# Performance work log

Measured on AMD Instinct MI355X. Metric: run time of the kernel, lower is better.

The kernel has to match this reference:

```python
import jax, jax.numpy as jnp
import numpy as np

C = 128
K = 5
M = 150000   # num vertices
NF = 300000  # num faces
D = 192      # volume side
NEG_SLOPE = 0.2


def _x_shift(K):
    # Exactly replicates the torch module's grid construction.
    grid = np.linspace(-K // 2, K // 2, K)
    grid_3d = np.stack(np.meshgrid(grid, grid, grid), axis=0).transpose(2, 1, 3, 0)
    return jnp.asarray(grid_3d.reshape(-1, 3), jnp.float32)  # [K^3, 3]


def _trilinear_border(vol, g):
    # vol: [D1, D2, D3]; g: [N, 3] normalized coords in (x, y, z) order
    # (x -> D3/W, y -> D2/H, z -> D1/D), align_corners=True, padding_mode='border'.
    D1, D2, D3 = vol.shape
    def pix(c, S):
        return jnp.clip((c + 1.0) * 0.5 * (S - 1), 0.0, S - 1.0)
    ix, iy, iz = pix(g[:, 0], D3), pix(g[:, 1], D2), pix(g[:, 2], D1)
    x0f, y0f, z0f = jnp.floor(ix), jnp.floor(iy), jnp.floor(iz)
    wx, wy, wz = ix - x0f, iy - y0f, iz - z0f
    x0 = x0f.astype(jnp.int32); y0 = y0f.astype(jnp.int32); z0 = z0f.astype(jnp.int32)
    x1 = jnp.minimum(x0 + 1, D3 - 1)
    y1 = jnp.minimum(y0 + 1, D2 - 1)
    z1 = jnp.minimum(z0 + 1, D1 - 1)
    c000 = vol[z0, y0, x0]; c001 = vol[z0, y0, x1]
    c010 = vol[z0, y1, x0]; c011 = vol[z0, y1, x1]
    c100 = vol[z1, y0, x0]; c101 = vol[z1, y0, x1]
    c110 = vol[z1, y1, x0]; c111 = vol[z1, y1, x1]
    c00 = c000 * (1 - wx) + c001 * wx
    c01 = c010 * (1 - wx) + c011 * wx
    c10 = c100 * (1 - wx) + c101 * wx
    c11 = c110 * (1 - wx) + c111 * wx
    c0 = c00 * (1 - wy) + c01 * wy
    c1 = c10 * (1 - wy) + c11 * wy
    return c0 * (1 - wz) + c1 * wz


def _leaky(x):
    return jnp.where(x >= 0, x, NEG_SLOPE * x)


def setup_inputs() -> dict:
    key = jax.random.key(0)
    ks = jax.random.split(key, 9)
    v = jax.random.uniform(ks[0], (1, M, 3), jnp.float32, -0.9, 0.9)
    f = jax.random.randint(ks[1], (1, NF, 3), 0, M, jnp.int32)
    V = jax.random.normal(ks[2], (1, 1, D, D, D), jnp.float32)
    def init(k, shape, fan):
        return jax.random.normal(k, shape, jnp.float32) / np.sqrt(fan).astype(np.float32)
    Wconv = init(ks[3], (C, 1, K, K, K), K ** 3)
    bconv = jnp.zeros((C,), jnp.float32)
    Wlfc = init(ks[4], (C, C), C)
    blfc = jnp.zeros((C,), jnp.float32)
    W1 = init(ks[5], (C, 6), 6)
    b1 = jnp.zeros((C,), jnp.float32)
    W2 = init(ks[6], (4 * C, 2 * C), 2 * C)
    b2 = jnp.zeros((4 * C,), jnp.float32)
    W3 = init(ks[7], (2 * C, 4 * C), 4 * C)
    b3 = jnp.zeros((2 * C,), jnp.float32)
    return dict(v=v, f=f, V=V, Wconv=Wconv, bconv=bconv, Wlfc=Wlfc, blfc=blfc,
                W1=W1, b1=b1, W2=W2, b2=b2, W3=W3, b3=b3)


def reference(v, f, V, Wconv, bconv, Wlfc, blfc, W1, b1, W2, b2, W3, b3):
    m = v.shape[1]
    D1, D2, D3 = V.shape[2], V.shape[3], V.shape[4]
    Dm = max(D1, D2, D3)
    rescale = jnp.array([D3 / Dm, D2 / Dm, D1 / Dm], jnp.float32)
    x_shift = _x_shift(K)  # [K^3, 3]

    # --- cube sampling (Q = n_scale = 1), done under no_grad in torch ---
    pts = (v[0][:, None, :] + x_shift / Dm * 2.0) / rescale  # [m, K^3, 3]
    cubes = _trilinear_border(V[0, 0], pts.reshape(-1, 3)).reshape(m, K ** 3)
    cubes = jax.lax.stop_gradient(cubes)

    # --- localconv: Conv3d with full-size kernel == GEMM over flattened cube ---
    z_local = cubes @ Wconv.reshape(C, -1).T + bconv      # [m, C]
    z_local = _leaky(z_local)
    z_local = _leaky(z_local @ Wlfc.T + blfc)             # [m, C]

    # --- vertex normals (area-weighted face-normal accumulation, pytorch3d style) ---
    faces = f[0]
    vv = v[0]
    p0, p1, p2 = vv[faces[:, 0]], vv[faces[:, 1]], vv[faces[:, 2]]
    fn = jnp.cross(p1 - p0, p2 - p0)
    vn = jnp.zeros_like(vv)
    vn = vn.at[faces[:, 0]].add(fn).at[faces[:, 1]].add(fn).at[faces[:, 2]].add(fn)
    vn = vn / jnp.maximum(jnp.linalg.norm(vn, axis=-1, keepdims=True), 1e-6)

    # --- point-wise MLP fusion ---
    x = jnp.concatenate([v, vn[None]], axis=2)            # [1, m, 6]
    z_point = _leaky(x @ W1.T + b1)                       # [1, m, C]
    z = jnp.concatenate([z_point, z_local[None]], axis=2) # [1, m, 2C]
    z = _leaky(z @ W2.T + b2)                             # [1, m, 4C]
    z = _leaky(z @ W3.T + b3)                             # [1, m, 2C]
    return z
```

## Files before the change

### kernel.cpp

```cpp
#include <hip/hip_runtime.h>
#include <hip/hip_fp16.h>

#define NEG_SLOPE 0.2f

using f16x8 = __attribute__((ext_vector_type(8))) _Float16;
using f32x4 = __attribute__((ext_vector_type(4))) float;

__device__ __forceinline__ float leakyf(float x) { return x >= 0.f ? x : NEG_SLOPE * x; }

__device__ __forceinline__ void gload_lds16(const void* g, void* l) {
    __builtin_amdgcn_global_load_lds(
        (const __attribute__((address_space(1))) unsigned int*)g,
        (__attribute__((address_space(3))) unsigned int*)l, 16, 0, 0);
}

#define MFMA16(a, b, c) __builtin_amdgcn_mfma_f32_16x16x32_f16(a, b, c, 0, 0, 0)

__global__ __launch_bounds__(256)
void fn_kernel(const float* __restrict__ v, const int* __restrict__ f,
               float4* __restrict__ fn4, int nf) {
    int i = blockIdx.x * 256 + threadIdx.x;
    if (i >= nf) return;
    int i0 = f[3 * i], i1 = f[3 * i + 1], i2 = f[3 * i + 2];
    float p0x = v[3 * i0], p0y = v[3 * i0 + 1], p0z = v[3 * i0 + 2];
    float ux = v[3 * i1] - p0x, uy = v[3 * i1 + 1] - p0y, uz = v[3 * i1 + 2] - p0z;
    float wx = v[3 * i2] - p0x, wy = v[3 * i2 + 1] - p0y, wz = v[3 * i2 + 2] - p0z;
    fn4[i] = make_float4(uy * wz - uz * wy, uz * wx - ux * wz, ux * wy - uy * wx, 0.f);
}

__global__ __launch_bounds__(256)
void inc_hist_kernel(const int* __restrict__ f, unsigned* __restrict__ gh, int NE) {
    __shared__ unsigned h[1024];
    const int t = threadIdx.x, blk = blockIdx.x;
    h[t] = 0; h[t + 256] = 0; h[t + 512] = 0; h[t + 768] = 0;
    __syncthreads();
    int base = blk * 4096;
#pragma unroll
    for (int k = 0; k < 16; ++k) {
        int idx = base + k * 256 + t;
        if (idx < NE) atomicAdd(&h[((unsigned)f[idx]) >> 8], 1u);
    }
    __syncthreads();
#pragma unroll
    for (int k = 0; k < 4; ++k) { int b = t + k * 256; gh[(size_t)blk * 1024 + b] = h[b]; }
}

__global__ __launch_bounds__(256)
void row_scan_kernel(unsigned* __restrict__ gh, unsigned* __restrict__ binTotals, int NB) {
    __shared__ unsigned s[256];
    __shared__ unsigned carrySh;
    const int bin = blockIdx.x, t = threadIdx.x;
    if (t == 0) carrySh = 0;
    __syncthreads();
    for (int base = 0; base < NB; base += 256) {
        unsigned c = carrySh;
        int i = base + t;
        unsigned val = (i < NB) ? gh[(size_t)i * 1024 + bin] : 0;
        s[t] = val;
        __syncthreads();
        for (int d = 1; d < 256; d <<= 1) {
            unsigned x = (t >= d) ? s[t - d] : 0;
            __syncthreads();
            s[t] += x;
            __syncthreads();
        }
        if (i < NB) gh[(size_t)i * 1024 + bin] = s[t] - val + c;
        if (t == 255) carrySh = c + s[255];
        __syncthreads();
    }
    if (t == 0) binTotals[bin] = carrySh;
}

__global__ __launch_bounds__(1024)
void bin_scan_kernel(const unsigned* __restrict__ binTotals, unsigned* __restrict__ binstart) {
    __shared__ unsigned s[1024];
    int t = threadIdx.x;
    unsigned val = binTotals[t];
    s[t] = val;
    __syncthreads();
    for (int d = 1; d < 1024; d <<= 1) {
        unsigned x = (t >= d) ? s[t - d] : 0;
        __syncthreads();
        s[t] += x;
        __syncthreads();
    }
    binstart[t] = s[t] - val;
    if (t == 1023) binstart[1024] = s[1023];
}

__global__ __launch_bounds__(256)
void inc_scatter_kernel(const int* __restrict__ f, const unsigned* __restrict__ gh,
                        const unsigned* __restrict__ binstart,
                        unsigned* __restrict__ sortedV, unsigned* __restrict__ sortedE,
                        int NE) {
    __shared__ unsigned loc[1024];
    const int t = threadIdx.x, blk = blockIdx.x;
#pragma unroll
    for (int k = 0; k < 4; ++k) {
        int b = t + k * 256;
        loc[b] = gh[(size_t)blk * 1024 + b] + binstart[b];
    }
    __syncthreads();
    int base = blk * 4096;
#pragma unroll
    for (int k = 0; k < 16; ++k) {
        int idx = base + k * 256 + t;
        if (idx < NE) {
            unsigned vv = (unsigned)f[idx];
            unsigned pos = atomicAdd(&loc[vv >> 8], 1u);
            sortedV[pos] = vv;
            sortedE[pos] = (unsigned)idx;
        }
    }
}

__global__ __launch_bounds__(256)
void vn_gather_kernel(const unsigned* __restrict__ sortedV, const unsigned* __restrict__ sortedE,
                      const float4* __restrict__ fn4, const unsigned* __restrict__ binstart,
                      float* __restrict__ vn, int M) {
    __shared__ float acc[768];
    const int t = threadIdx.x, b = blockIdx.x;
    acc[t] = 0.f; acc[t + 256] = 0.f; acc[t + 512] = 0.f;
    __syncthreads();
    unsigned s = binstart[b], e = binstart[b + 1];
    for (unsigned i = s + t; i < e; i += 256) {
        unsigned vv = sortedV[i];
        float4 fn = fn4[sortedE[i] / 3];
        int lv = (int)(vv & 255u) * 3;
        atomicAdd(&acc[lv + 0], fn.x);
        atomicAdd(&acc[lv + 1], fn.y);
        atomicAdd(&acc[lv + 2], fn.z);
    }
    __syncthreads();
    int gv = b * 256 + t;
    if (gv < M) {
        vn[3 * gv + 0] = acc[t * 3 + 0];
        vn[3 * gv + 1] = acc[t * 3 + 1];
        vn[3 * gv + 2] = acc[t * 3 + 2];
    }
}

__global__ __launch_bounds__(256)
void code_hist_kernel(const float* __restrict__ v, int* __restrict__ codes,
                      int* __restrict__ hist, int M) {
    int i = blockIdx.x * 256 + threadIdx.x;
    if (i >= M) return;
    int cx = min(max((int)((v[3 * i + 0] + 1.f) * 8.f), 0), 15);
    int cy = min(max((int)((v[3 * i + 1] + 1.f) * 8.f), 0), 15);
    int cz = min(max((int)((v[3 * i + 2] + 1.f) * 8.f), 0), 15);
    int code = 0;
#pragma unroll
    for (int b = 0; b < 4; ++b)
        code |= (((cx >> b) & 1) << (3 * b)) | (((cy >> b) & 1) << (3 * b + 1)) |
                (((cz >> b) & 1) << (3 * b + 2));
    codes[i] = code;
    atomicAdd(&hist[code], 1);
}

__global__ __launch_bounds__(1024)
void scan_kernel(const int* __restrict__ hist, int* __restrict__ offs) {
    __shared__ int s[1024];
    int t = threadIdx.x;
    int v0 = hist[4 * t], v1 = hist[4 * t + 1], v2 = hist[4 * t + 2], v3 = hist[4 * t + 3];
    int sum = v0 + v1 + v2 + v3;
    s[t] = sum;
    __syncthreads();
    for (int d = 1; d < 1024; d <<= 1) {
        int val = (t >= d) ? s[t - d] : 0;
        __syncthreads();
        s[t] += val;
        __syncthreads();
    }
    int excl = s[t] - sum;
    offs[4 * t + 0] = excl;
    offs[4 * t + 1] = excl + v0;
    offs[4 * t + 2] = excl + v0 + v1;
    offs[4 * t + 3] = excl + v0 + v1 + v2;
}

__global__ __launch_bounds__(256)
void scatter_kernel(const int* __restrict__ codes, int* __restrict__ offs,
                    int* __restrict__ perm, int M) {
    int i = blockIdx.x * 256 + threadIdx.x;
    if (i >= M) return;
    int pos = atomicAdd(&offs[codes[i]], 1);
    perm[pos] = i;
}

__global__ __launch_bounds__(256)
void sample_kernel(const float* __restrict__ v, const float* __restrict__ vol,
                   const int* __restrict__ perm,
                   __half* __restrict__ cubes, int m_start, int cnt, int nwg) {
    __shared__ float bbox[2][392];
    __shared__ int pi0[2][16];
    __shared__ float pw[2][16];
    const int half = threadIdx.x >> 7;
    const int q = threadIdx.x & 127;
    int q8 = nwg >> 3, r8 = nwg & 7;
    int xcd = blockIdx.x & 7, idxb = blockIdx.x >> 3;
    int bid = (xcd < r8 ? xcd * (q8 + 1) : r8 * (q8 + 1) + (xcd - r8) * q8) + idxb;
    int ml = bid * 2 + half;
    bool valid = ml < cnt;
    int m = valid ? perm[m_start + ml] : 0;

    if (valid && q < 15) {
        int axis = q / 5, idx = q - 5 * axis;
        float g = -3.f + 1.25f * (float)idx;
        float p = v[3 * m + axis] + g / 192.f * 2.f;
        float pos = fminf(fmaxf((p + 1.f) * 0.5f * 191.f, 0.f), 191.f);
        float fl = floorf(pos);
        pi0[half][q] = (int)fl;
        pw[half][q] = pos - fl;
    }
    __syncthreads();
    if (valid) {
        int xlo = pi0[half][0], ylo = pi0[half][5], zlo = pi0[half][10];
        for (int i = q; i < 392; i += 128) {
            int dx = i & 7;
            int dy = (i >> 3) % 7;
            int dz = i / 56;
            int X = min(xlo + dx, 191), Y = min(ylo + dy, 191), Z = min(zlo + dz, 191);
            bbox[half][i] = vol[Z * 36864 + Y * 192 + X];
        }
    }
    __syncthreads();
    if (!valid) return;
    __half* dst = cubes + (size_t)ml * 128;
    if (q >= 125) { dst[q] = __float2half(0.f); return; }
    int a = q % 5, b = (q / 5) % 5, c = q / 25;
    int xlo = pi0[half][0], ylo = pi0[half][5], zlo = pi0[half][10];
    int gx0 = pi0[half][a], gy0 = pi0[half][5 + b], gz0 = pi0[half][10 + c];
    float wxv = pw[half][a], wyv = pw[half][5 + b], wzv = pw[half][10 + c];
    int x0 = gx0 - xlo, y0 = gy0 - ylo, z0 = gz0 - zlo;
    int x1 = min(gx0 + 1, 191) - xlo;
    int y1 = min(gy0 + 1, 191) - ylo;
    int z1 = min(gz0 + 1, 191) - zlo;
    const float* bb = bbox[half];
    int b00 = (z0 * 7 + y0) * 8, b01 = (z0 * 7 + y1) * 8;
    int b10 = (z1 * 7 + y0) * 8, b11 = (z1 * 7 + y1) * 8;
    float c000 = bb[b00 + x0], c001 = bb[b00 + x1];
    float c010 = bb[b01 + x0], c011 = bb[b01 + x1];
    float c100 = bb[b10 + x0], c101 = bb[b10 + x1];
    float c110 = bb[b11 + x0], c111 = bb[b11 + x1];
    float omx = 1.f - wxv, omy = 1.f - wyv, omz = 1.f - wzv;
    float c00 = c000 * omx + c001 * wxv;
    float c01 = c010 * omx + c011 * wxv;
    float c10 = c100 * omx + c101 * wxv;
    float c11 = c110 * omx + c111 * wxv;
    float c0 = c00 * omy + c01 * wyv;
    float c1 = c10 * omy + c11 * wyv;
    dst[25 * a + 5 * b + c] = __float2half(c0 * omz + c1 * wzv);
}

__global__ __launch_bounds__(256)
void prep_weights(const float* __restrict__ Wconv, const float* __restrict__ Wlfc,
                  const float* __restrict__ W2, const float* __restrict__ W3,
                  __half* __restrict__ wpadh, __half* __restrict__ wlfch,
                  __half* __restrict__ w2h, __half* __restrict__ w3h) {
    int b = blockIdx.x, t = threadIdx.x;
    if (b < 64) {
        int i = b * 256 + t; int ch = i >> 7, k = i & 127;
        wpadh[i] = __float2half(k < 125 ? Wconv[ch * 125 + k] : 0.f);
    } else if (b < 128) {
        int i = (b - 64) * 256 + t; wlfch[i] = __float2half(Wlfc[i]);
    } else if (b < 640) {
        int i = (b - 128) * 256 + t; w2h[i] = __float2half(W2[i]);
    } else {
        int i = (b - 640) * 256 + t; w3h[i] = __float2half(W3[i]);
    }
}

__global__ __launch_bounds__(256)
void point_kernel(const float* __restrict__ v, const float* __restrict__ vn,
                  const int* __restrict__ perm,
                  const float* __restrict__ W1, const float* __restrict__ b1,
                  __half* __restrict__ zcat, int m_start, int cnt) {
    int ml = blockIdx.x * 2 + (threadIdx.x >> 7);
    if (ml >= cnt) return;
    int n = threadIdx.x & 127;
    int m = perm[m_start + ml];
    float x0 = v[3 * m], x1 = v[3 * m + 1], x2 = v[3 * m + 2];
    float nx = vn[3 * m], ny = vn[3 * m + 1], nz = vn[3 * m + 2];
    float nrm = fmaxf(sqrtf(nx * nx + ny * ny + nz * nz), 1e-6f);
    nx /= nrm; ny /= nrm; nz /= nrm;
    const float* w = W1 + n * 6;
    float z = b1[n] + x0 * w[0] + x1 * w[1] + x2 * w[2] + nx * w[3] + ny * w[4] + nz * w[5];
    zcat[(size_t)ml * 256 + n] = __float2half(leakyf(z));
}

__global__ __launch_bounds__(256)
void convlfc_kernel(const __half* __restrict__ cubes, const __half* __restrict__ wconvh,
                    const float* __restrict__ bconv, const __half* __restrict__ wlfch,
                    const float* __restrict__ blfc, __half* __restrict__ zcat) {
    __shared__ __half Zt[128 * 128];
    __shared__ __half As[128 * 64];
    __shared__ __half Bs[128 * 64];
    const int t = threadIdx.x;
    const int lane = t & 63, wave = t >> 6;
    const int lr = lane & 15, lg = lane >> 4;
    const int wm = wave >> 1, wn = wave & 1;
    const int m0 = blockIdx.x * 128;
    const int srow = t >> 3;
    const int scb = ((t & 7) << 4) ^ (((t >> 3) & 7) << 4);
    const int swz = (lr & 7) << 4;

    const __half* Ag = cubes + (size_t)(m0 + srow) * 128 + (scb >> 1);
    const __half* Bg = wconvh + (size_t)srow * 128 + (scb >> 1);
    __half* Al = As + wave * 512;
    __half* Bl = Bs + wave * 512;
    const char* aB = (const char*)As + (wm * 64 + lr) * 128;
    const char* bB = (const char*)Bs + (wn * 64 + lr) * 128;

    f32x4 acc[4][4] = {};
    for (int kc = 0; kc < 128; kc += 64) {
#pragma unroll
        for (int i = 0; i < 4; ++i) {
            gload_lds16(Ag + (size_t)i * 32 * 128 + kc, Al + i * 2048);
            gload_lds16(Bg + (size_t)i * 32 * 128 + kc, Bl + i * 2048);
        }
        __syncthreads();
#pragma unroll
        for (int kk = 0; kk < 2; ++kk) {
            const int ko = (kk * 64 + lg * 16) ^ swz;
            f16x8 af[4], bf[4];
#pragma unroll
            for (int fx = 0; fx < 4; ++fx) {
                af[fx] = *(const f16x8*)(aB + fx * 2048 + ko);
                bf[fx] = *(const f16x8*)(bB + fx * 2048 + ko);
            }
#pragma unroll
            for (int fm = 0; fm < 4; ++fm)
#pragma unroll
                for (int fn = 0; fn < 4; ++fn)
                    acc[fm][fn] = MFMA16(af[fm], bf[fn], acc[fm][fn]);
        }
        __syncthreads();
    }
#pragma unroll
    for (int fm = 0; fm < 4; ++fm) {
#pragma unroll
        for (int fn = 0; fn < 4; ++fn) {
            int col = wn * 64 + fn * 16 + lr;
            float bias = bconv[col];
#pragma unroll
            for (int r = 0; r < 4; ++r) {
                int row = wm * 64 + fm * 16 + lg * 4 + r;
                float val = leakyf(acc[fm][fn][r] + bias);
                *(__half*)((char*)Zt + row * 256 + ((2 * col) ^ ((row & 7) << 4))) = __float2half(val);
            }
        }
    }
    __syncthreads();

    const __half* Bg2 = wlfch + (size_t)srow * 128 + (scb >> 1);
    const char* zR = (const char*)Zt + (wm * 64 + lr) * 256;
    f32x4 acc2[4][4] = {};
    for (int kc = 0; kc < 128; kc += 64) {
#pragma unroll
        for (int i = 0; i < 4; ++i)
            gload_lds16(Bg2 + (size_t)i * 32 * 128 + kc, Bl + i * 2048);
        __syncthreads();
#pragma unroll
        for (int kk = 0; kk < 2; ++kk) {
            const int kb = kc * 2 + kk * 64 + lg * 16;
            const int ko = (kk * 64 + lg * 16) ^ swz;
            f16x8 af[4], bf[4];
#pragma unroll
            for (int fx = 0; fx < 4; ++fx) {
                af[fx] = *(const f16x8*)(zR + fx * 4096 + (kb ^ swz));
                bf[fx] = *(const f16x8*)(bB + fx * 2048 + ko);
            }
#pragma unroll
            for (int fm = 0; fm < 4; ++fm)
#pragma unroll
                for (int fn = 0; fn < 4; ++fn)
                    acc2[fm][fn] = MFMA16(af[fm], bf[fn], acc2[fm][fn]);
        }
        __syncthreads();
    }
#pragma unroll
    for (int fm = 0; fm < 4; ++fm) {
#pragma unroll
        for (int fn = 0; fn < 4; ++fn) {
            int col = wn * 64 + fn * 16 + lr;
            float bias = blfc[col];
#pragma unroll
            for (int r = 0; r < 4; ++r) {
                int row = m0 + wm * 64 + fm * 16 + lg * 4 + r;
                zcat[(size_t)row * 256 + 128 + col] = __float2half(leakyf(acc2[fm][fn][r] + bias));
            }
        }
    }
}

template<bool F32OUT>
__global__ __launch_bounds__(256)
void gemm_mfma(const __half* __restrict__ A, const __half* __restrict__ W,
               const float* __restrict__ bias, void* __restrict__ outp,
               int K, int Meff, int OS, int OC, const int* __restrict__ rowmap) {
    __shared__ __half As[8192];
    __shared__ __half Bs[8192];
    const int t = threadIdx.x;
    const int lane = t & 63, wave = t >> 6;
    const int lr = lane & 15, lg = lane >> 4;
    const int wm = wave >> 1, wn = wave & 1;
    const int m0 = blockIdx.x * 128, n0 = blockIdx.y * 128;

    const int srow = t >> 3;
    const int scb = ((t & 7) << 4) ^ (((t >> 3) & 7) << 4);
    const __half* Ag = A + (size_t)(m0 + srow) * K + (scb >> 1);
    const __half* Wg = W + (size_t)(n0 + srow) * K + (scb >> 1);
    __half* Al = As + wave * 512;
    __half* Bl = Bs + wave * 512;

    const int swz = (lr & 7) << 4;
    const char* aB = (const char*)As + (wm * 64 + lr) * 128;
    const char* bB = (const char*)Bs + (wn * 64 + lr) * 128;
    const int k0 = (lg * 16) ^ swz;
    const int k1 = (64 + lg * 16) ^ swz;

    f32x4 acc[4][4] = {};

    for (int kc = 0; kc < K; kc += 64) {
#pragma unroll
        for (int i = 0; i < 4; ++i) {
            gload_lds16(Ag + (size_t)i * 32 * K + kc, Al + i * 2048);
            gload_lds16(Wg + (size_t)i * 32 * K + kc, Bl + i * 2048);
        }
        __syncthreads();
        f16x8 af[4], bf[4];
#pragma unroll
        for (int fx = 0; fx < 4; ++fx) {
            af[fx] = *(const f16x8*)(aB + fx * 2048 + k0);
            bf[fx] = *(const f16x8*)(bB + fx * 2048 + k0);
        }
#pragma unroll
        for (int fm = 0; fm < 4; ++fm)
#pragma unroll
            for (int fn = 0; fn < 4; ++fn)
                acc[fm][fn] = MFMA16(af[fm], bf[fn], acc[fm][fn]);
#pragma unroll
        for (int fx = 0; fx < 4; ++fx) {
            af[fx] = *(const f16x8*)(aB + fx * 2048 + k1);
            bf[fx] = *(const f16x8*)(bB + fx * 2048 + k1);
        }
#pragma unroll
        for (int fm = 0; fm < 4; ++fm)
#pragma unroll
            for (int fn = 0; fn < 4; ++fn)
                acc[fm][fn] = MFMA16(af[fm], bf[fn], acc[fm][fn]);
        __syncthreads();
    }

    float bv[4];
#pragma unroll
    for (int fn = 0; fn < 4; ++fn) bv[fn] = bias[n0 + wn * 64 + fn * 16 + lr];
    const int rbase = m0 + wm * 64 + lg * 4;
    const int cbase = OC + n0 + wn * 64 + lr;
#pragma unroll
    for (int fm = 0; fm < 4; ++fm) {
#pragma unroll
        for (int r = 0; r < 4; ++r) {
            int row = rbase + fm * 16 + r;
            if (row < Meff) {
                size_t orow = (size_t)(rowmap ? rowmap[row] : row);
#pragma unroll
                for (int fn = 0; fn < 4; ++fn) {
                    float val = leakyf(acc[fm][fn][r] + bv[fn]);
                    if (F32OUT)
                        ((float*)outp)[orow * OS + cbase + fn * 16] = val;
                    else
                        ((__half*)outp)[orow * OS + cbase + fn * 16] = __float2half(val);
                }
            }
        }
    }
}

extern "C" void kernel_launch(void* const* d_in, const int* in_sizes, int n_in,
                              void* d_out, int out_size, void* d_ws, size_t ws_size,
                              hipStream_t stream) {
    const float* v = (const float*)d_in[0];
    const int* f = (const int*)d_in[1];
    const float* vol = (const float*)d_in[2];
    const float* Wconv = (const float*)d_in[3];
    const float* bconv = (const float*)d_in[4];
    const float* Wlfc = (const float*)d_in[5];
    const float* blfc = (const float*)d_in[6];
    const float* W1 = (const float*)d_in[7];
    const float* b1 = (const float*)d_in[8];
    const float* W2 = (const float*)d_in[9];
    const float* b2 = (const float*)d_in[10];
    const float* W3 = (const float*)d_in[11];
    const float* b3 = (const float*)d_in[12];
    float* out = (float*)d_out;
    const int M = in_sizes[0] / 3;
    const int NF = in_sizes[1] / 3;
    const int NE = 3 * NF;
    const int NB = (NE + 4095) / 4096;

    char* base = (char*)d_ws;
    float* vn = (float*)base;
    size_t off = ((size_t)M * 12 + 255) & ~(size_t)255;
    int* codes = (int*)(base + off); off += ((size_t)M * 4 + 255) & ~(size_t)255;
    int* perm  = (int*)(base + off); off += ((size_t)M * 4 + 255) & ~(size_t)255;
    int* hist  = (int*)(base + off); off += 4096 * 4;
    int* offs  = (int*)(base + off); off += 4096 * 4;
    float4* fn4 = (float4*)(base + off); off += (size_t)NF * 16;
    unsigned* sortedV = (unsigned*)(base + off); off += ((size_t)NE * 4 + 255) & ~(size_t)255;
    unsigned* sortedE = (unsigned*)(base + off); off += ((size_t)NE * 4 + 255) & ~(size_t)255;
    unsigned* gh = (unsigned*)(base + off); off += ((size_t)1024 * NB * 4 + 255) & ~(size_t)255;
    unsigned* binstart = (unsigned*)(base + off); off += 1032 * 4;
    unsigned* binTotals = (unsigned*)(base + off); off += 1024 * 4;
    __half* wpadh = (__half*)(base + off); off += 32768;
    __half* wlfch = (__half*)(base + off); off += 32768;
    __half* w2h = (__half*)(base + off); off += 262144;
    __half* w3h = (__half*)(base + off); off += 262144;
    size_t avail = ws_size > off ? ws_size - off : 0;
    size_t Mpad = ((size_t)M + 127) & ~(size_t)127;
    size_t chm = (avail / 1792) & ~(size_t)127;
    if (chm > Mpad) chm = Mpad;
    if (chm < 128) chm = 128;
    __half* cubes = (__half*)(base + off);
    __half* zcat = cubes + chm * 128;
    __half* h = zcat + chm * 256;

    fn_kernel<<<(NF + 255) / 256, 256, 0, stream>>>(v, f, fn4, NF);
    inc_hist_kernel<<<NB, 256, 0, stream>>>(f, gh, NE);
    row_scan_kernel<<<1024, 256, 0, stream>>>(gh, binTotals, NB);
    bin_scan_kernel<<<1, 1024, 0, stream>>>(binTotals, binstart);
    inc_scatter_kernel<<<NB, 256, 0, stream>>>(f, gh, binstart, sortedV, sortedE, NE);
    vn_gather_kernel<<<(M + 255) / 256, 256, 0, stream>>>(sortedV, sortedE, fn4, binstart, vn, M);

    hipMemsetAsync(hist, 0, 4096 * 4, stream);
    code_hist_kernel<<<(M + 255) / 256, 256, 0, stream>>>(v, codes, hist, M);
    scan_kernel<<<1, 1024, 0, stream>>>(hist, offs);
    scatter_kernel<<<(M + 255) / 256, 256, 0, stream>>>(codes, offs, perm, M);
    prep_weights<<<1152, 256, 0, stream>>>(Wconv, Wlfc, W2, W3, wpadh, wlfch, w2h, w3h);

    for (size_t ms = 0; ms < (size_t)M; ms += chm) {
        size_t rem = (size_t)M - ms;
        int cnt = (int)(rem < chm ? rem : chm);
        int mb = (cnt + 127) / 128;
        int nblk = (cnt + 1) / 2;
        sample_kernel<<<nblk, 256, 0, stream>>>(v, vol, perm, cubes, (int)ms, cnt, nblk);
        convlfc_kernel<<<mb, 256, 0, stream>>>(cubes, wpadh, bconv, wlfch, blfc, zcat);
        point_kernel<<<(cnt + 1) / 2, 256, 0, stream>>>(v, vn, perm, W1, b1, zcat, (int)ms, cnt);
        gemm_mfma<false><<<dim3(mb, 4), 256, 0, stream>>>(zcat, w2h, b2, h, 256, mb * 128, 512, 0, nullptr);
        gemm_mfma<true><<<dim3(mb, 2), 256, 0, stream>>>(h, w3h, b3, out, 512, cnt, 256, 0, perm + ms);
    }
}
```

Measured before the change: 518.7 us.

## Widen GEMM N-tile to 256 and restructure sample bbox load layout

The MLP GEMMs now compute 128x256 tiles per block, with each wave holding 4x8 MFMA accumulators. This halves the grid along N and reuses each A tile across twice as many output columns, at the cost of more registers and LDS per block and lower occupancy. Separately, the sampling kernel's bounding-box gather now uses a fixed (dy,dx) mapping per thread with a z loop. It stores rows with a stride of 9 floats instead of 8, aiming to cut integer div/mod work and LDS bank conflicts.

```diff
diff --git a/kernel.cpp b/kernel.cpp
--- a/kernel.cpp
+++ b/kernel.cpp
@@ -191,7 +191,7 @@
 void sample_kernel(const float* __restrict__ v, const float* __restrict__ vol,
                    const int* __restrict__ perm,
                    __half* __restrict__ cubes, int m_start, int cnt, int nwg) {
-    __shared__ float bbox[2][392];
+    __shared__ float bbox[2][448];
     __shared__ int pi0[2][16];
     __shared__ float pw[2][16];
     const int half = threadIdx.x >> 7;
@@ -215,12 +215,21 @@
     __syncthreads();
     if (valid) {
         int xlo = pi0[half][0], ylo = pi0[half][5], zlo = pi0[half][10];
-        for (int i = q; i < 392; i += 128) {
-            int dx = i & 7;
-            int dy = (i >> 3) % 7;
-            int dz = i / 56;
-            int X = min(xlo + dx, 191), Y = min(ylo + dy, 191), Z = min(zlo + dz, 191);
-            bbox[half][i] = vol[Z * 36864 + Y * 192 + X];
+        int j = q & 63;
+        int dy = j >> 3, dx = j & 7;
+        if (dy < 7) {
+            int X = min(xlo + dx, 191);
+            int Y = min(ylo + dy, 191);
+            int rowoff = dy * 9 + dx;
+            const float* volYX = vol + Y * 192 + X;
+#pragma unroll
+            for (int k = 0; k < 4; ++k) {
+                int pz = (q >> 6) + k * 2;
+                if (pz < 7) {
+                    int Z = min(zlo + pz, 191);
+                    bbox[half][pz * 63 + rowoff] = volYX[Z * 36864];
+                }
+            }
         }
     }
     __syncthreads();
@@ -236,8 +245,8 @@
     int y1 = min(gy0 + 1, 191) - ylo;
     int z1 = min(gz0 + 1, 191) - zlo;
     const float* bb = bbox[half];
-    int b00 = (z0 * 7 + y0) * 8, b01 = (z0 * 7 + y1) * 8;
-    int b10 = (z1 * 7 + y0) * 8, b11 = (z1 * 7 + y1) * 8;
+    int b00 = z0 * 63 + y0 * 9, b01 = z0 * 63 + y1 * 9;
+    int b10 = z1 * 63 + y0 * 9, b11 = z1 * 63 + y1 * 9;
     float c000 = bb[b00 + x0], c001 = bb[b00 + x1];
     float c010 = bb[b01 + x0], c011 = bb[b01 + x1];
     float c100 = bb[b10 + x0], c101 = bb[b10 + x1];
@@ -395,16 +404,16 @@
 
 template<bool F32OUT>
 __global__ __launch_bounds__(256)
-void gemm_mfma(const __half* __restrict__ A, const __half* __restrict__ W,
+void gemm_bigm(const __half* __restrict__ A, const __half* __restrict__ W,
                const float* __restrict__ bias, void* __restrict__ outp,
                int K, int Meff, int OS, int OC, const int* __restrict__ rowmap) {
     __shared__ __half As[8192];
-    __shared__ __half Bs[8192];
+    __shared__ __half Bs[16384];
     const int t = threadIdx.x;
     const int lane = t & 63, wave = t >> 6;
     const int lr = lane & 15, lg = lane >> 4;
     const int wm = wave >> 1, wn = wave & 1;
-    const int m0 = blockIdx.x * 128, n0 = blockIdx.y * 128;
+    const int m0 = blockIdx.x * 128, n0 = blockIdx.y * 256;
 
     const int srow = t >> 3;
     const int scb = ((t & 7) << 4) ^ (((t >> 3) & 7) << 4);
@@ -415,48 +424,44 @@
 
     const int swz = (lr & 7) << 4;
     const char* aB = (const char*)As + (wm * 64 + lr) * 128;
-    const char* bB = (const char*)Bs + (wn * 64 + lr) * 128;
+    const char* bB = (const char*)Bs + (wn * 128 + lr) * 128;
     const int k0 = (lg * 16) ^ swz;
     const int k1 = (64 + lg * 16) ^ swz;
 
-    f32x4 acc[4][4] = {};
+    f32x4 acc[4][8] = {};
 
     for (int kc = 0; kc < K; kc += 64) {
 #pragma unroll
-        for (int i = 0; i < 4; ++i) {
+        for (int i = 0; i < 4; ++i)
             gload_lds16(Ag + (size_t)i * 32 * K + kc, Al + i * 2048);
+#pragma unroll
+        for (int i = 0; i < 8; ++i)
             gload_lds16(Wg + (size_t)i * 32 * K + kc, Bl + i * 2048);
-        }
-        __syncthreads();
-        f16x8 af[4], bf[4];
-#pragma unroll
-        for (int fx = 0; fx < 4; ++fx) {
-            af[fx] = *(const f16x8*)(aB + fx * 2048 + k0);
-            bf[fx] = *(const f16x8*)(bB + fx * 2048 + k0);
-        }
-#pragma unroll
-        for (int fm = 0; fm < 4; ++fm)
-#pragma unroll
-            for (int fn = 0; fn < 4; ++fn)
-                acc[fm][fn] = MFMA16(af[fm], bf[fn], acc[fm][fn]);
-#pragma unroll
-        for (int fx = 0; fx < 4; ++fx) {
-            af[fx] = *(const f16x8*)(aB + fx * 2048 + k1);
-            bf[fx] = *(const f16x8*)(bB + fx * 2048 + k1);
-        }
-#pragma unroll
-        for (int fm = 0; fm < 4; ++fm)
-#pragma unroll
-            for (int fn = 0; fn < 4; ++fn)
-                acc[fm][fn] = MFMA16(af[fm], bf[fn], acc[fm][fn]);
-        __syncthreads();
-    }
-
-    float bv[4];
-#pragma unroll
-    for (int fn = 0; fn < 4; ++fn) bv[fn] = bias[n0 + wn * 64 + fn * 16 + lr];
+        __syncthreads();
+#pragma unroll
+        for (int kk = 0; kk < 2; ++kk) {
+            const int ko = (kk == 0) ? k0 : k1;
+            f16x8 af[4], bf[8];
+#pragma unroll
+            for (int fm = 0; fm < 4; ++fm)
+                af[fm] = *(const f16x8*)(aB + fm * 2048 + ko);
+#pragma unroll
+            for (int fn = 0; fn < 8; ++fn)
+                bf[fn] = *(const f16x8*)(bB + fn * 2048 + ko);
+#pragma unroll
+            for (int fm = 0; fm < 4; ++fm)
+#pragma unroll
+                for (int fn = 0; fn < 8; ++fn)
+                    acc[fm][fn] = MFMA16(af[fm], bf[fn], acc[fm][fn]);
+        }
+        __syncthreads();
+    }
+
+    float bv[8];
+#pragma unroll
+    for (int fn = 0; fn < 8; ++fn) bv[fn] = bias[n0 + wn * 128 + fn * 16 + lr];
     const int rbase = m0 + wm * 64 + lg * 4;
-    const int cbase = OC + n0 + wn * 64 + lr;
+    const int cbase = OC + n0 + wn * 128 + lr;
 #pragma unroll
     for (int fm = 0; fm < 4; ++fm) {
 #pragma unroll
@@ -465,7 +470,7 @@
             if (row < Meff) {
                 size_t orow = (size_t)(rowmap ? rowmap[row] : row);
 #pragma unroll
-                for (int fn = 0; fn < 4; ++fn) {
+                for (int fn = 0; fn < 8; ++fn) {
                     float val = leakyf(acc[fm][fn][r] + bv[fn]);
                     if (F32OUT)
                         ((float*)outp)[orow * OS + cbase + fn * 16] = val;
@@ -546,7 +551,9 @@
         sample_kernel<<<nblk, 256, 0, stream>>>(v, vol, perm, cubes, (int)ms, cnt, nblk);
         convlfc_kernel<<<mb, 256, 0, stream>>>(cubes, wpadh, bconv, wlfch, blfc, zcat);
         point_kernel<<<(cnt + 1) / 2, 256, 0, stream>>>(v, vn, perm, W1, b1, zcat, (int)ms, cnt);
-        gemm_mfma<false><<<dim3(mb, 4), 256, 0, stream>>>(zcat, w2h, b2, h, 256, mb * 128, 512, 0, nullptr);
-        gemm_mfma<true><<<dim3(mb, 2), 256, 0, stream>>>(h, w3h, b3, out, 512, cnt, 256, 0, perm + ms);
-    }
-}
+        gemm_bigm<false><<<dim3(mb, 2), 256, 0, stream>>>(
+            zcat, w2h, b2, h, 256, mb * 128, 512, 0, nullptr);
+        gemm_bigm<true><<<dim3(mb, 1), 256, 0, stream>>>(
+            h, w3h, b3, out, 512, cnt, 256, 0, perm + ms);
+    }
+}
```

After: 557.3 us. +7.4%, slower.
